# Kernel tuning notes

Hardware: AMD Instinct MI355X
Metric: run time of the kernel (lower is better)

The kernel has to match this reference:

```python
import jax, jax.numpy as jnp
import numpy as np

N_NODES = 50000

def _gcn_layer(x, src, dst, W, b, n_nodes):
    # x: [N, F_in]; src/dst: [E+N] (self-loops already appended)
    h = x @ W  # [N, F_out]
    deg = jax.ops.segment_sum(jnp.ones_like(dst, dtype=h.dtype), dst, num_segments=n_nodes)
    dinv = jnp.where(deg > 0, jax.lax.rsqrt(deg), 0.0)  # deg^{-1/2}
    norm = dinv[src] * dinv[dst]  # [E+N]
    msg = h[src] * norm[:, None]  # gather + scale
    out = jax.ops.segment_sum(msg, dst, num_segments=n_nodes)  # scatter-add
    return out + b

def setup_inputs() -> dict:
    key = jax.random.key(0)
    k1, k2, k3, k4 = jax.random.split(key, 4)
    d = 128
    E = 800000
    x = jax.random.normal(k1, (N_NODES, d), dtype=jnp.float32)
    edge_index = jax.random.randint(k2, (2, E), 0, N_NODES, dtype=jnp.int64)
    W1 = jax.random.normal(k3, (d, d), dtype=jnp.float32) / np.sqrt(d)
    b1 = jnp.zeros((d,), dtype=jnp.float32)
    W2 = jax.random.normal(k4, (d, d), dtype=jnp.float32) / np.sqrt(d)
    b2 = jnp.zeros((d,), dtype=jnp.float32)
    return {"x": x, "edge_index": edge_index, "W1": W1, "b1": b1, "W2": W2, "b2": b2}

def reference(x, edge_index, W1, b1, W2, b2):
    n = x.shape[0]
    loops = jnp.arange(n, dtype=edge_index.dtype)
    src = jnp.concatenate([edge_index[0], loops])  # add self-loops
    dst = jnp.concatenate([edge_index[1], loops])
    h = _gcn_layer(x, src, dst, W1, b1, n)
    h = jax.nn.relu(h)
    z = _gcn_layer(h, src, dst, W2, b2, n)
    return z
```

## Files before the change

kernel.cpp:

```cpp
#include <hip/hip_runtime.h>
#include <hip/hip_fp16.h>

#define NF 128
#define KC 64
#define NPART 4
#define NPMAX 12544

typedef _Float16 half8  __attribute__((ext_vector_type(8)));
typedef _Float16 half4v __attribute__((ext_vector_type(4)));
typedef float    floatx4 __attribute__((ext_vector_type(4)));

__global__ __launch_bounds__(512) void count2_k(
    const int* __restrict__ dst, unsigned char* __restrict__ pcnt,
    int E, int N, int Ec)
{
    __shared__ int lcnt[NPMAX];
    const int p = blockIdx.x & 3, c = blockIdx.x >> 2;
    const int Np = (N + 3) >> 2;
    const int lo = p * Np, hi = min(lo + Np, N);
    const int sz = hi - lo;
    for (int i = threadIdx.x; i < sz; i += 512) lcnt[i] = 0;
    __syncthreads();

    const int e0 = c * Ec, e1 = min(e0 + Ec, E);
    for (int e = e0 + (int)threadIdx.x * 4; e + 3 < e1; e += 512 * 4) {
        int4 d = *(const int4*)(dst + e);
        if (d.x >= lo && d.x < hi) atomicAdd(&lcnt[d.x - lo], 1);
        if (d.y >= lo && d.y < hi) atomicAdd(&lcnt[d.y - lo], 1);
        if (d.z >= lo && d.z < hi) atomicAdd(&lcnt[d.z - lo], 1);
        if (d.w >= lo && d.w < hi) atomicAdd(&lcnt[d.w - lo], 1);
    }
    int rem0 = e0 + ((e1 - e0) & ~3);
    for (int e = rem0 + (int)threadIdx.x; e < e1; e += 512) {
        int d = dst[e];
        if (d >= lo && d < hi) atomicAdd(&lcnt[d - lo], 1);
    }
    __syncthreads();
    for (int i = threadIdx.x; i < sz; i += 512)
        pcnt[(size_t)c * N + lo + i] = (unsigned char)lcnt[i];
}

__global__ __launch_bounds__(256) void pscan2_k(
    unsigned char* __restrict__ pcnt, float* __restrict__ dinv,
    int* __restrict__ rowptr, int* __restrict__ blocksum, int n, int N, int nb,
    const float* __restrict__ W1, const float* __restrict__ W2,
    __half* __restrict__ WT1, __half* __restrict__ WT2)
{
    if ((int)blockIdx.x >= nb) {
        int idx = ((int)blockIdx.x - nb) * 256 + threadIdx.x;
        const float* W = (idx < 16384) ? W1 : W2;
        __half* WT     = (idx < 16384) ? WT1 : WT2;
        int j = idx & 16383;
        int nn = j & 127, k = j >> 7;
        WT[nn * NF + k] = __float2half(W[k * NF + nn]);
        return;
    }
    __shared__ int sm[256];
    int tid = threadIdx.x;
    int bin = blockIdx.x * 256 + tid;
    int total = 0;
    if (bin < n) {
        #pragma unroll 4
        for (int c = 0; c < KC; c++) {
            size_t o = (size_t)c * N + bin;
            int v = pcnt[o];
            pcnt[o] = (unsigned char)total;
            total += v;
        }
        dinv[bin] = rsqrtf((float)total + 1.0f);
    }
    sm[tid] = total;
    __syncthreads();
    #pragma unroll
    for (int d = 1; d < 256; d <<= 1) {
        int t = (tid >= d) ? sm[tid - d] : 0;
        __syncthreads();
        sm[tid] += t;
        __syncthreads();
    }
    if (bin < n) rowptr[bin] = sm[tid] - total;
    if (tid == 255) blocksum[blockIdx.x] = sm[255];
}

template<bool F32IN>
__device__ __forceinline__ void gemm_body512(
    const void* __restrict__ Xv, const __half* __restrict__ WT,
    const float* __restrict__ dinv, __half* __restrict__ out, int M, int bid,
    __half (*wlds)[136])
{
    const int tid = threadIdx.x;
    {
        int r = tid >> 2;
        int c0 = (tid & 3) * 32;
        const half8* s = (const half8*)(WT + (size_t)r * NF + c0);
        half8* d = (half8*)&wlds[r][c0];
        #pragma unroll
        for (int j = 0; j < 4; j++) d[j] = s[j];
    }
    __syncthreads();

    const int wave = tid >> 6, lane = tid & 63;
    const int quad = lane >> 4, l15 = lane & 15;
    const int rowA = bid * 128 + wave * 16 + l15;
    const int rowc = (rowA < M) ? rowA : (M - 1);

    half8 afr[4];
    if (F32IN) {
        const float* X = (const float*)Xv;
        #pragma unroll
        for (int kc = 0; kc < 4; kc++) {
            const floatx4* p = (const floatx4*)(X + (size_t)rowc * NF + kc * 32 + quad * 8);
            floatx4 u = p[0], v = p[1];
            half8 a;
            a[0] = (_Float16)u[0]; a[1] = (_Float16)u[1];
            a[2] = (_Float16)u[2]; a[3] = (_Float16)u[3];
            a[4] = (_Float16)v[0]; a[5] = (_Float16)v[1];
            a[6] = (_Float16)v[2]; a[7] = (_Float16)v[3];
            afr[kc] = a;
        }
    } else {
        const __half* X = (const __half*)Xv;
        #pragma unroll
        for (int kc = 0; kc < 4; kc++)
            afr[kc] = *(const half8*)(X + (size_t)rowc * NF + kc * 32 + quad * 8);
    }

    floatx4 acc[8];
    #pragma unroll
    for (int ct = 0; ct < 8; ct++) { floatx4 z = {0.f, 0.f, 0.f, 0.f}; acc[ct] = z; }

    #pragma unroll
    for (int kc = 0; kc < 4; kc++) {
        #pragma unroll
        for (int ct = 0; ct < 8; ct++) {
            half8 b = *(const half8*)&wlds[ct * 16 + l15][kc * 32 + quad * 8];
            acc[ct] = __builtin_amdgcn_mfma_f32_16x16x32_f16(afr[kc], b, acc[ct], 0, 0, 0);
        }
    }

    const int orow0 = bid * 128 + wave * 16 + quad * 4;
    #pragma unroll
    for (int r = 0; r < 4; r++) {
        int orow = orow0 + r;
        if (orow < M) {
            float s = dinv[orow];
            #pragma unroll
            for (int ct = 0; ct < 8; ct++)
                out[(size_t)orow * NF + ct * 16 + l15] = __float2half(acc[ct][r] * s);
        }
    }
}

__global__ __launch_bounds__(512) void mid_k(
    const int* __restrict__ src, const int* __restrict__ dst,
    const int* __restrict__ rowptr, const unsigned char* __restrict__ coff,
    const int* __restrict__ blocksum, int* __restrict__ rowptr2,
    int* __restrict__ csr, int E, int N, int Ec, int nb,
    const float* __restrict__ X, const __half* __restrict__ WT,
    const float* __restrict__ dinv, __half* __restrict__ H, int GB2)
{
    __shared__ __align__(16) char smem[NPMAX * 4 + 1024];
    const int tid = threadIdx.x;
    if ((int)blockIdx.x < GB2) {
        gemm_body512<true>(X, WT, dinv, H, N, blockIdx.x, (__half(*)[136])smem);
        return;
    }
    int* lcur = (int*)smem;
    int* pref = (int*)(smem + NPMAX * 4);

    const int b = blockIdx.x - GB2;
    const int p = b & 3, c = b >> 2;
    const int Np = (N + 3) >> 2;
    const int lo = p * Np, hi = min(lo + Np, N);
    const int sz = hi - lo;

    int v = (tid < nb) ? blocksum[tid] : 0;
    if (tid < 256) pref[tid] = v;
    __syncthreads();
    #pragma unroll
    for (int d = 1; d < 256; d <<= 1) {
        int t = (tid < 256 && tid >= d) ? pref[tid - d] : 0;
        __syncthreads();
        if (tid < 256) pref[tid] += t;
        __syncthreads();
    }
    if (tid < 256) pref[tid] -= v;
    __syncthreads();

    for (int i = tid; i < sz; i += 512) {
        int bin = lo + i;
        int r = rowptr[bin] + pref[bin >> 8] + (int)coff[(size_t)c * N + bin];
        lcur[i] = r;
        if (c == 0) rowptr2[bin] = r;
    }
    if (c == 0 && p == 0 && tid == 0) rowptr2[N] = E;
    __syncthreads();

    const int e0 = c * Ec, e1 = min(e0 + Ec, E);
    for (int e = e0 + tid * 4; e + 3 < e1; e += 512 * 4) {
        int4 d = *(const int4*)(dst + e);
        int4 s = *(const int4*)(src + e);
        if (d.x >= lo && d.x < hi) csr[atomicAdd(&lcur[d.x - lo], 1)] = s.x;
        if (d.y >= lo && d.y < hi) csr[atomicAdd(&lcur[d.y - lo], 1)] = s.y;
        if (d.z >= lo && d.z < hi) csr[atomicAdd(&lcur[d.z - lo], 1)] = s.z;
        if (d.w >= lo && d.w < hi) csr[atomicAdd(&lcur[d.w - lo], 1)] = s.w;
    }
    int rem0 = e0 + ((e1 - e0) & ~3);
    for (int e = rem0 + tid; e < e1; e += 512) {
        int d = dst[e];
        if (d >= lo && d < hi) csr[atomicAdd(&lcur[d - lo], 1)] = src[e];
    }
}

__global__ __launch_bounds__(256) void gemm2_k(
    const __half* __restrict__ A, const __half* __restrict__ WT,
    const float* __restrict__ dinv, __half* __restrict__ H, int M)
{
    __shared__ __half wlds[128][136];
    const int tid = threadIdx.x;
    {
        int r = tid >> 1, c0 = (tid & 1) * 64;
        const half8* s = (const half8*)(WT + (size_t)r * NF + c0);
        half8* d = (half8*)&wlds[r][c0];
        #pragma unroll
        for (int j = 0; j < 8; j++) d[j] = s[j];
    }
    __syncthreads();

    const int wave = tid >> 6, lane = tid & 63;
    const int quad = lane >> 4, l15 = lane & 15;
    const int rowA = blockIdx.x * 64 + wave * 16 + l15;
    const int rowc = (rowA < M) ? rowA : (M - 1);

    half8 afr[4];
    #pragma unroll
    for (int kc = 0; kc < 4; kc++)
        afr[kc] = *(const half8*)(A + (size_t)rowc * NF + kc * 32 + quad * 8);

    floatx4 acc[8];
    #pragma unroll
    for (int ct = 0; ct < 8; ct++) { floatx4 z = {0.f, 0.f, 0.f, 0.f}; acc[ct] = z; }

    #pragma unroll
    for (int kc = 0; kc < 4; kc++) {
        #pragma unroll
        for (int ct = 0; ct < 8; ct++) {
            half8 b = *(const half8*)&wlds[ct * 16 + l15][kc * 32 + quad * 8];
            acc[ct] = __builtin_amdgcn_mfma_f32_16x16x32_f16(afr[kc], b, acc[ct], 0, 0, 0);
        }
    }

    const int orow0 = blockIdx.x * 64 + wave * 16 + quad * 4;
    #pragma unroll
    for (int r = 0; r < 4; r++) {
        int orow = orow0 + r;
        if (orow < M) {
            float s = dinv[orow];
            #pragma unroll
            for (int ct = 0; ct < 8; ct++)
                H[(size_t)orow * NF + ct * 16 + l15] = __float2half(acc[ct][r] * s);
        }
    }
}

__device__ __forceinline__ floatx4 gather_acc(
    const half4v* __restrict__ hs4, const int* __restrict__ csr,
    int base, int cnt, int node, int eg, int fl, int lane)
{
    floatx4 acc = {0.f, 0.f, 0.f, 0.f};
    int m0 = min(64, cnt);
    int idx0 = 0;
    if (lane < m0) idx0 = __builtin_nontemporal_load(&csr[base + lane]);
    if (eg == 0) {
        half4v s = hs4[(size_t)node * 32 + fl];
        acc[0] = (float)s[0]; acc[1] = (float)s[1];
        acc[2] = (float)s[2]; acc[3] = (float)s[3];
    }
    for (int off = 0; off < cnt; off += 64) {
        int m = min(64, cnt - off);
        int idx = (off == 0) ? idx0 : 0;
        if (off && lane < m) idx = __builtin_nontemporal_load(&csr[base + off + lane]);
        for (int j = 0; j < m; j += 16) {
            int s[8];
            half4v v[8];
            #pragma unroll
            for (int t = 0; t < 8; t++)
                s[t] = __shfl(idx, min(j + 2 * t + eg, m - 1), 64);
            #pragma unroll
            for (int t = 0; t < 8; t++)
                v[t] = hs4[(size_t)s[t] * 32 + fl];
            #pragma unroll
            for (int t = 0; t < 8; t++) {
                if (j + 2 * t + eg < m) {
                    acc[0] += (float)v[t][0]; acc[1] += (float)v[t][1];
                    acc[2] += (float)v[t][2]; acc[3] += (float)v[t][3];
                }
            }
        }
    }
    #pragma unroll
    for (int k = 0; k < 4; k++) acc[k] += __shfl_xor(acc[k], 32, 64);
    return acc;
}

__global__ __launch_bounds__(256) void agg_k(
    const __half* __restrict__ hs, const int* __restrict__ rowptr,
    const int* __restrict__ csr, const float* __restrict__ dinv,
    const float* __restrict__ bias, __half* __restrict__ outh,
    float* __restrict__ outf, int n)
{
    int wave = threadIdx.x >> 6;
    int lane = threadIdx.x & 63;
    int node = blockIdx.x * 4 + wave;
    if (node >= n) return;
    const int eg = lane >> 5, fl = lane & 31;

    int base = rowptr[node];
    int cnt  = rowptr[node + 1] - base;
    floatx4 acc = gather_acc((const half4v*)hs, csr, base, cnt, node, eg, fl, lane);

    if (eg == 0) {
        float dv = dinv[node];
        float o0 = dv * acc[0] + bias[fl * 4 + 0];
        float o1 = dv * acc[1] + bias[fl * 4 + 1];
        float o2 = dv * acc[2] + bias[fl * 4 + 2];
        float o3 = dv * acc[3] + bias[fl * 4 + 3];
        if (outh) {
            half4v h;
            h[0] = (_Float16)fmaxf(o0, 0.f); h[1] = (_Float16)fmaxf(o1, 0.f);
            h[2] = (_Float16)fmaxf(o2, 0.f); h[3] = (_Float16)fmaxf(o3, 0.f);
            *(half4v*)&outh[(size_t)node * NF + fl * 4] = h;
        } else {
            floatx4 w = {o0, o1, o2, o3};
            *(floatx4*)(outf + (size_t)node * NF + fl * 4) = w;
        }
    }
}


extern "C" void kernel_launch(void* const* d_in, const int* in_sizes, int n_in,
                              void* d_out, int out_size, void* d_ws, size_t ws_size,
                              hipStream_t stream) {
    const float* x  = (const float*)d_in[0];
    const int*   ei = (const int*)d_in[1];
    const float* W1 = (const float*)d_in[2];
    const float* b1 = (const float*)d_in[3];
    const float* W2 = (const float*)d_in[4];
    const float* b2 = (const float*)d_in[5];
    float* out = (float*)d_out;

    const int N = in_sizes[0] / NF;
    const int E = in_sizes[1] / 2;
    const int* src = ei;
    const int* dst = ei + E;

    char* ws = (char*)d_ws;
    size_t off = 0;
    auto alloc = [&](size_t bytes) {
        void* p = ws + off;
        off += bytes;
        off = (off + 63) & ~(size_t)63;
        return p;
    };
    unsigned char* pcnt = (unsigned char*)alloc((size_t)KC * N);
    int*    rowptr  = (int*)alloc((size_t)(N + 1) * 4);
    int*    rowptr2 = (int*)alloc((size_t)(N + 1) * 4);
    int*    csr     = (int*)alloc((size_t)E * 4);
    float*  dinv    = (float*)alloc((size_t)N * 4);
    int*    bsum    = (int*)alloc((size_t)256 * 4);
    __half* WT1     = (__half*)alloc((size_t)NF * NF * 2);
    __half* WT2     = (__half*)alloc((size_t)NF * NF * 2);
    __half* H16     = (__half*)alloc((size_t)N * NF * 2);
    __half* A16     = (__half*)alloc((size_t)N * NF * 2);

    int nb  = (N + 255) / 256;
    int Ec  = (((E + KC - 1) / KC) + 3) & ~3;
    int GB2 = (N + 127) / 128;
    int gb  = (N + 63) / 64;
    int ab  = (N + 3) / 4;

    count2_k<<<KC * NPART, 512, 0, stream>>>(dst, pcnt, E, N, Ec);
    pscan2_k<<<nb + 128, 256, 0, stream>>>(pcnt, dinv, rowptr, bsum, N, N, nb,
                                           W1, W2, WT1, WT2);
    mid_k<<<GB2 + KC * NPART, 512, 0, stream>>>(src, dst, rowptr, pcnt, bsum,
                                                rowptr2, csr, E, N, Ec, nb,
                                                x, WT1, dinv, H16, GB2);
    agg_k<<<ab, 256, 0, stream>>>(H16, rowptr2, csr, dinv, b1, A16, nullptr, N);
    gemm2_k<<<gb, 256, 0, stream>>>(A16, WT2, dinv, H16, N);
    agg_k<<<ab, 256, 0, stream>>>(H16, rowptr2, csr, dinv, b2, nullptr, out, N);
}
```

Baseline: 208.5 us.

## Fuse first-layer aggregation with second-layer GEMM into one kernel

Replaces the separate layer-1 aggregation kernel and the layer-2 GEMM kernel with a single kernel. Each block aggregates 16 nodes into shared memory, applies bias and ReLU, then multiplies by W2 with MFMA and writes the dinv-scaled result. This removes one launch and the global round trip of the intermediate activation. In exchange, each block does only 16 rows, W2 fragments are read from global or cache per block rather than staged in LDS, and the block's four waves (four nodes each) must all finish before the GEMM stage starts.

Measured after the change: 206.9 us. About the same (-0.8%).

```diff
diff --git a/kernel.cpp b/kernel.cpp
--- a/kernel.cpp
+++ b/kernel.cpp
@@ -209,57 +209,6 @@
     for (int e = rem0 + tid; e < e1; e += 512) {
         int d = dst[e];
         if (d >= lo && d < hi) csr[atomicAdd(&lcur[d - lo], 1)] = src[e];
-    }
-}
-
-__global__ __launch_bounds__(256) void gemm2_k(
-    const __half* __restrict__ A, const __half* __restrict__ WT,
-    const float* __restrict__ dinv, __half* __restrict__ H, int M)
-{
-    __shared__ __half wlds[128][136];
-    const int tid = threadIdx.x;
-    {
-        int r = tid >> 1, c0 = (tid & 1) * 64;
-        const half8* s = (const half8*)(WT + (size_t)r * NF + c0);
-        half8* d = (half8*)&wlds[r][c0];
-        #pragma unroll
-        for (int j = 0; j < 8; j++) d[j] = s[j];
-    }
-    __syncthreads();
-
-    const int wave = tid >> 6, lane = tid & 63;
-    const int quad = lane >> 4, l15 = lane & 15;
-    const int rowA = blockIdx.x * 64 + wave * 16 + l15;
-    const int rowc = (rowA < M) ? rowA : (M - 1);
-
-    half8 afr[4];
-    #pragma unroll
-    for (int kc = 0; kc < 4; kc++)
-        afr[kc] = *(const half8*)(A + (size_t)rowc * NF + kc * 32 + quad * 8);
-
-    floatx4 acc[8];
-    #pragma unroll
-    for (int ct = 0; ct < 8; ct++) { floatx4 z = {0.f, 0.f, 0.f, 0.f}; acc[ct] = z; }
-
-    #pragma unroll
-    for (int kc = 0; kc < 4; kc++) {
-        #pragma unroll
-        for (int ct = 0; ct < 8; ct++) {
-            half8 b = *(const half8*)&wlds[ct * 16 + l15][kc * 32 + quad * 8];
-            acc[ct] = __builtin_amdgcn_mfma_f32_16x16x32_f16(afr[kc], b, acc[ct], 0, 0, 0);
-        }
-    }
-
-    const int orow0 = blockIdx.x * 64 + wave * 16 + quad * 4;
-    #pragma unroll
-    for (int r = 0; r < 4; r++) {
-        int orow = orow0 + r;
-        if (orow < M) {
-            float s = dinv[orow];
-            #pragma unroll
-            for (int ct = 0; ct < 8; ct++)
-                H[(size_t)orow * NF + ct * 16 + l15] = __float2half(acc[ct][r] * s);
-        }
     }
 }
 
@@ -337,6 +286,70 @@
     }
 }
 
+__global__ __launch_bounds__(256) void aggmm_k(
+    const __half* __restrict__ hs, const int* __restrict__ rowptr,
+    const int* __restrict__ csr, const float* __restrict__ dinv,
+    const float* __restrict__ bias, const __half* __restrict__ WT,
+    __half* __restrict__ Hout, int n)
+{
+    __shared__ __half alds[16][136];
+    const int tid = threadIdx.x;
+    const int wave = tid >> 6, lane = tid & 63;
+    const int eg = lane >> 5, fl = lane & 31;
+    const int nb0 = blockIdx.x * 16;
+
+    #pragma unroll 1
+    for (int q = 0; q < 4; q++) {
+        int node = nb0 + wave * 4 + q;
+        if (node < n) {
+            int base = rowptr[node];
+            int cnt  = rowptr[node + 1] - base;
+            floatx4 acc = gather_acc((const half4v*)hs, csr, base, cnt, node, eg, fl, lane);
+            if (eg == 0) {
+                float dv = dinv[node];
+                half4v h;
+                h[0] = (_Float16)fmaxf(dv * acc[0] + bias[fl * 4 + 0], 0.f);
+                h[1] = (_Float16)fmaxf(dv * acc[1] + bias[fl * 4 + 1], 0.f);
+                h[2] = (_Float16)fmaxf(dv * acc[2] + bias[fl * 4 + 2], 0.f);
+                h[3] = (_Float16)fmaxf(dv * acc[3] + bias[fl * 4 + 3], 0.f);
+                *(half4v*)&alds[wave * 4 + q][fl * 4] = h;
+            }
+        } else if (eg == 0) {
+            half4v z = {(_Float16)0.f, (_Float16)0.f, (_Float16)0.f, (_Float16)0.f};
+            *(half4v*)&alds[wave * 4 + q][fl * 4] = z;
+        }
+    }
+    __syncthreads();
+
+    const int quad = lane >> 4, l15 = lane & 15;
+    half8 afr[4];
+    #pragma unroll
+    for (int kc = 0; kc < 4; kc++)
+        afr[kc] = *(const half8*)&alds[l15][kc * 32 + quad * 8];
+
+    floatx4 acc0 = {0.f, 0.f, 0.f, 0.f};
+    floatx4 acc1 = {0.f, 0.f, 0.f, 0.f};
+    const int ct0 = wave * 2, ct1 = wave * 2 + 1;
+    #pragma unroll
+    for (int kc = 0; kc < 4; kc++) {
+        half8 b0 = *(const half8*)(WT + (size_t)(ct0 * 16 + l15) * NF + kc * 32 + quad * 8);
+        half8 b1 = *(const half8*)(WT + (size_t)(ct1 * 16 + l15) * NF + kc * 32 + quad * 8);
+        acc0 = __builtin_amdgcn_mfma_f32_16x16x32_f16(afr[kc], b0, acc0, 0, 0, 0);
+        acc1 = __builtin_amdgcn_mfma_f32_16x16x32_f16(afr[kc], b1, acc1, 0, 0, 0);
+    }
+
+    #pragma unroll
+    for (int r = 0; r < 4; r++) {
+        int row = quad * 4 + r;
+        int node = nb0 + row;
+        if (node < n) {
+            float s = dinv[node];
+            Hout[(size_t)node * NF + ct0 * 16 + l15] = __float2half(acc0[r] * s);
+            Hout[(size_t)node * NF + ct1 * 16 + l15] = __float2half(acc1[r] * s);
+        }
+    }
+}
+
 
 extern "C" void kernel_launch(void* const* d_in, const int* in_sizes, int n_in,
                               void* d_out, int out_size, void* d_ws, size_t ws_size,
@@ -376,7 +389,7 @@
     int nb  = (N + 255) / 256;
     int Ec  = (((E + KC - 1) / KC) + 3) & ~3;
     int GB2 = (N + 127) / 128;
-    int gb  = (N + 63) / 64;
+    int fb  = (N + 15) / 16;
     int ab  = (N + 3) / 4;
 
     count2_k<<<KC * NPART, 512, 0, stream>>>(dst, pcnt, E, N, Ec);
@@ -385,7 +398,6 @@
     mid_k<<<GB2 + KC * NPART, 512, 0, stream>>>(src, dst, rowptr, pcnt, bsum,
                                                 rowptr2, csr, E, N, Ec, nb,
                                                 x, WT1, dinv, H16, GB2);
-    agg_k<<<ab, 256, 0, stream>>>(H16, rowptr2, csr, dinv, b1, A16, nullptr, N);
-    gemm2_k<<<gb, 256, 0, stream>>>(A16, WT2, dinv, H16, N);
-    agg_k<<<ab, 256, 0, stream>>>(H16, rowptr2, csr, dinv, b2, nullptr, out, N);
-}
+    aggmm_k<<<fb, 256, 0, stream>>>(H16, rowptr2, csr, dinv, b1, WT2, A16, N);
+    agg_k<<<ab, 256, 0, stream>>>(A16, rowptr2, csr, dinv, b2, nullptr, out, N);
+}
```
